# Kernel optimization log

Measured on AMD Instinct MI355X. Metric: run time of the kernel, lower is better.

Reference implementation:

```python
import jax, jax.numpy as jnp
import numpy as np

Q_DIM = 2048
HEADS = 16
HEAD_DIM = 128
INNER = HEADS * HEAD_DIM          # 2048
MLP_HID = int(Q_DIM * 4.0)        # 8192
MLP_MULT = 2
EPS = 1e-05
B, S = 2, 2048


def setup_inputs() -> dict:
    key = jax.random.key(0)
    ks = jax.random.split(key, 4)
    hidden_states = jax.random.normal(ks[0], (B, S, Q_DIM), dtype=jnp.float32)
    # interleaved RoPE tables: cos/sin of shape [S, HEAD_DIM]
    half = HEAD_DIM // 2
    freqs = 1.0 / (10000.0 ** (np.arange(half, dtype=np.float64) / half))
    ang = np.outer(np.arange(S, dtype=np.float64), freqs)      # [S, half]
    ang = np.repeat(ang, 2, axis=-1)                            # [S, HEAD_DIM]
    rope_cos = jnp.asarray(np.cos(ang), dtype=jnp.float32)
    rope_sin = jnp.asarray(np.sin(ang), dtype=jnp.float32)
    fused_out = 3 * INNER + MLP_HID * MLP_MULT                  # 22528
    W_qkv_mlp = jax.random.normal(ks[1], (Q_DIM, fused_out), dtype=jnp.float32) * (Q_DIM ** -0.5)
    norm_q_w = jnp.ones((HEAD_DIM,), dtype=jnp.float32)
    norm_k_w = jnp.ones((HEAD_DIM,), dtype=jnp.float32)
    W_out = jax.random.normal(ks[2], (INNER + MLP_HID, Q_DIM), dtype=jnp.float32) * ((INNER + MLP_HID) ** -0.5)
    b_out = jnp.zeros((Q_DIM,), dtype=jnp.float32)
    return {"hidden_states": hidden_states, "rope_cos": rope_cos, "rope_sin": rope_sin,
            "W_qkv_mlp": W_qkv_mlp, "norm_q_w": norm_q_w, "norm_k_w": norm_k_w,
            "W_out": W_out, "b_out": b_out}


def _rms_norm(x, w):
    # RMSNorm over the last (head_dim) axis
    return x * jax.lax.rsqrt(jnp.mean(x * x, axis=-1, keepdims=True) + EPS) * w


def _apply_rope(x, cos, sin):
    # x: [B, S, H, D]; interleaved rotate-half (diffusers real-rope convention)
    xr = x.reshape(*x.shape[:-1], HEAD_DIM // 2, 2)
    rot = jnp.stack([-xr[..., 1], xr[..., 0]], axis=-1).reshape(x.shape)
    return x * cos[None, :, None, :] + rot * sin[None, :, None, :]


def reference(hidden_states, rope_cos, rope_sin, W_qkv_mlp, norm_q_w, norm_k_w, W_out, b_out):
    b, s, _ = hidden_states.shape
    proj = hidden_states @ W_qkv_mlp                              # [B,S,22528]
    qkv, mlp_h = jnp.split(proj, [3 * INNER], axis=-1)
    q, k, v = jnp.split(qkv, 3, axis=-1)
    q = q.reshape(b, s, HEADS, HEAD_DIM)
    k = k.reshape(b, s, HEADS, HEAD_DIM)
    v = v.reshape(b, s, HEADS, HEAD_DIM)
    q = _rms_norm(q, norm_q_w)
    k = _rms_norm(k, norm_k_w)
    q = _apply_rope(q, rope_cos, rope_sin)
    k = _apply_rope(k, rope_cos, rope_sin)
    scale = HEAD_DIM ** -0.5
    scores = jnp.einsum('bqhd,bkhd->bhqk', q, k) * scale          # [B,H,S,S]
    attn = jax.nn.softmax(scores, axis=-1)
    out_attn = jnp.einsum('bhqk,bkhd->bqhd', attn, v).reshape(b, s, INNER)
    m1, m2 = jnp.split(mlp_h, 2, axis=-1)                         # SwiGLU
    mlp_out = jax.nn.silu(m1) * m2                                # [B,S,MLP_HID]
    cat = jnp.concatenate([out_attn, mlp_out], axis=-1)           # [B,S,INNER+MLP_HID]
    return cat @ W_out + b_out
```

## Files before the change

kernel.cpp:

```cpp
#include <hip/hip_runtime.h>

typedef unsigned short u16;
typedef unsigned int u32;
typedef __bf16 bf16x8 __attribute__((ext_vector_type(8)));
typedef float f32x4 __attribute__((ext_vector_type(4)));

#define MFMA16(a, b, c) __builtin_amdgcn_mfma_f32_16x16x32_bf16((a), (b), (c), 0, 0, 0)

#define S_LEN 2048
#define D_HEAD 128
#define NHEADS 16
#define NBH 32
#define QDIM 2048
#define NPROJ 22528
#define NCAT 10240
#define MROWS 4096

__device__ __forceinline__ float bf2f(u16 u) { return __uint_as_float(((u32)u) << 16); }
__device__ __forceinline__ u16 f2bf(float f) {
  u32 u = __float_as_uint(f);
  return (u16)((u + 0x7FFFu + ((u >> 16) & 1u)) >> 16);
}
__device__ __forceinline__ void gld16(const void* g, void* l) {
  __builtin_amdgcn_global_load_lds((__attribute__((address_space(1))) void*)(g),
                                   (__attribute__((address_space(3))) void*)(l), 16, 0, 0);
}

__global__ __launch_bounds__(256) void f32_to_bf16(const float* __restrict__ in,
                                                   u16* __restrict__ out) {
  const u32 i = blockIdx.x * 256 + threadIdx.x;
  const float4 v = ((const float4*)in)[i];
  uint2 o;
  o.x = (u32)f2bf(v.x) | ((u32)f2bf(v.y) << 16);
  o.y = (u32)f2bf(v.z) | ((u32)f2bf(v.w) << 16);
  ((uint2*)out)[i] = o;
}

__global__ __launch_bounds__(256) void transpose_f32_bf16(const float* __restrict__ in,
                                                          u16* __restrict__ out, int R, int C) {
  __shared__ u16 tile[64][65];
  const int tx = threadIdx.x & 63;
  const int ty = threadIdx.x >> 6;
  const int c0 = blockIdx.x * 64;
  const int r0 = blockIdx.y * 64;
#pragma unroll
  for (int it = 0; it < 16; ++it) {
    const int rr = ty * 16 + it;
    tile[rr][tx] = f2bf(in[(size_t)(r0 + rr) * C + c0 + tx]);
  }
  __syncthreads();
#pragma unroll
  for (int it = 0; it < 16; ++it) {
    const int rr = ty * 16 + it;
    out[(size_t)(c0 + rr) * R + r0 + tx] = tile[tx][rr];
  }
}

__global__ __launch_bounds__(256) void transpose_bf16_b(const u16* __restrict__ in,
                                                        u16* __restrict__ out, int R, int C) {
  __shared__ u16 tile[64][65];
  const int z = blockIdx.z;
  in += (size_t)z * R * C;
  out += (size_t)z * R * C;
  const int tx = threadIdx.x & 63;
  const int ty = threadIdx.x >> 6;
  const int c0 = blockIdx.x * 64;
  const int r0 = blockIdx.y * 64;
#pragma unroll
  for (int it = 0; it < 16; ++it) {
    const int rr = ty * 16 + it;
    tile[rr][tx] = in[(size_t)(r0 + rr) * C + c0 + tx];
  }
  __syncthreads();
#pragma unroll
  for (int it = 0; it < 16; ++it) {
    const int rr = ty * 16 + it;
    out[(size_t)(c0 + rr) * R + r0 + tx] = tile[tx][rr];
  }
}

template <int OUTF32>
__global__ __launch_bounds__(256, 2) void gemm_bt(const u16* __restrict__ A,
                                                  const u16* __restrict__ Bt,
                                                  void* __restrict__ Cvoid,
                                                  const float* __restrict__ bias, int N, int K) {
  __shared__ u16 As[128 * 64];
  __shared__ u16 Bs[128 * 64];
  const int t = threadIdx.x;
  const int l = t & 63;
  const int w = t >> 6;
  const int lr = l & 15;
  const int lg = l >> 4;
  const int m0 = blockIdx.y * 128;
  const int n0 = blockIdx.x * 128;
  const int wm = (w >> 1) * 64;
  const int wn = (w & 1) * 64;

  f32x4 acc[4][4] = {};
  const int obase = w * 1024 + l * 16;

  for (int k0 = 0; k0 < K; k0 += 64) {
#pragma unroll
    for (int rnd = 0; rnd < 4; ++rnd) {
      const int o = obase + rnd * 4096;
      const int row = o >> 7;
      const int g = (o & 127) >> 4;
      const int gs = g ^ (row & 7);
      gld16(A + (size_t)(m0 + row) * K + k0 + gs * 8, &As[rnd * 2048 + w * 512]);
      gld16(Bt + (size_t)(n0 + row) * K + k0 + gs * 8, &Bs[rnd * 2048 + w * 512]);
    }
    __syncthreads();

    bf16x8 af[4][2], bfr[4][2];
#pragma unroll
    for (int i = 0; i < 4; ++i) {
#pragma unroll
      for (int kc = 0; kc < 2; ++kc) {
        const int ra = wm + i * 16 + lr;
        af[i][kc] = *(const bf16x8*)&As[ra * 64 + (((kc * 4 + lg) ^ (ra & 7)) * 8)];
        const int rb = wn + i * 16 + lr;
        bfr[i][kc] = *(const bf16x8*)&Bs[rb * 64 + (((kc * 4 + lg) ^ (rb & 7)) * 8)];
      }
    }
#pragma unroll
    for (int kc = 0; kc < 2; ++kc)
#pragma unroll
      for (int i = 0; i < 4; ++i)
#pragma unroll
        for (int j = 0; j < 4; ++j)
          acc[i][j] = MFMA16(af[i][kc], bfr[j][kc], acc[i][j]);
    __syncthreads();
  }

  if (OUTF32) {
    float* C = (float*)Cvoid;
#pragma unroll
    for (int i = 0; i < 4; ++i)
#pragma unroll
      for (int j = 0; j < 4; ++j)
#pragma unroll
        for (int r = 0; r < 4; ++r) {
          const int row = m0 + wm + i * 16 + lg * 4 + r;
          const int col = n0 + wn + j * 16 + lr;
          C[(size_t)row * N + col] = acc[i][j][r] + bias[col];
        }
  } else {
    u16* C = (u16*)Cvoid;
#pragma unroll
    for (int i = 0; i < 4; ++i)
#pragma unroll
      for (int j = 0; j < 4; ++j)
#pragma unroll
        for (int r = 0; r < 4; ++r) {
          const int row = m0 + wm + i * 16 + lg * 4 + r;
          const int col = n0 + wn + j * 16 + lr;
          C[(size_t)row * N + col] = f2bf(acc[i][j][r]);
        }
  }
}

__global__ __launch_bounds__(256) void norm_rope(const u16* __restrict__ proj,
                                                 const float* __restrict__ cosT,
                                                 const float* __restrict__ sinT,
                                                 const float* __restrict__ wq,
                                                 const float* __restrict__ wk,
                                                 u16* __restrict__ Qb, u16* __restrict__ Kb,
                                                 u16* __restrict__ Vb) {
  const int l = threadIdx.x & 63;
  const int wg = blockIdx.x * 4 + (threadIdx.x >> 6);
  const int h = wg & 15;
  const int r = wg >> 4;
  const int b = r >> 11;
  const int s = r & 2047;
  const int bh = (b << 4) + h;

  const u16* p = proj + (size_t)r * NPROJ + h * 128 + 2 * l;
  const u32 qu = *(const u32*)(p);
  const u32 ku = *(const u32*)(p + QDIM);
  const u32 vu = *(const u32*)(p + 2 * QDIM);

  const float q0 = bf2f(qu & 0xffff), q1 = bf2f(qu >> 16);
  const float k0 = bf2f(ku & 0xffff), k1 = bf2f(ku >> 16);

  float sq = q0 * q0 + q1 * q1;
  float sk = k0 * k0 + k1 * k1;
#pragma unroll
  for (int m = 1; m < 64; m <<= 1) {
    sq += __shfl_xor(sq, m);
    sk += __shfl_xor(sk, m);
  }
  const float scq = rsqrtf(sq * (1.0f / 128.0f) + 1e-5f);
  const float sck = rsqrtf(sk * (1.0f / 128.0f) + 1e-5f);

  const float2 cc = *(const float2*)&cosT[s * 128 + 2 * l];
  const float2 ssn = *(const float2*)&sinT[s * 128 + 2 * l];
  const float w0 = wq[2 * l], w1 = wq[2 * l + 1];
  const float x0 = wk[2 * l], x1 = wk[2 * l + 1];

  const float qn0 = q0 * scq * w0, qn1 = q1 * scq * w1;
  const float kn0 = k0 * sck * x0, kn1 = k1 * sck * x1;

  const float ATT = 0.08838834764831845f;
  const float qr0 = (qn0 * cc.x - qn1 * ssn.x) * ATT;
  const float qr1 = (qn1 * cc.y + qn0 * ssn.y) * ATT;
  const float kr0 = kn0 * cc.x - kn1 * ssn.x;
  const float kr1 = kn1 * cc.y + kn0 * ssn.y;

  const size_t dst = ((size_t)bh * S_LEN + s) * 128 + 2 * l;
  *(u32*)(Qb + dst) = (u32)f2bf(qr0) | ((u32)f2bf(qr1) << 16);
  *(u32*)(Kb + dst) = (u32)f2bf(kr0) | ((u32)f2bf(kr1) << 16);
  *(u32*)(Vb + dst) = vu;
}

__global__ __launch_bounds__(256) void swiglu(const u16* __restrict__ proj,
                                              u16* __restrict__ Cat) {
  const u32 i = blockIdx.x * 256 + threadIdx.x;
  const u32 r = i >> 11;
  const u32 c = (i & 2047) * 4;
  const u16* p1 = proj + (size_t)r * NPROJ + 3 * QDIM + c;
  const uint2 a = *(const uint2*)p1;
  const uint2 bv = *(const uint2*)(p1 + 8192);
  const float a0 = bf2f(a.x & 0xffff), a1 = bf2f(a.x >> 16);
  const float a2 = bf2f(a.y & 0xffff), a3 = bf2f(a.y >> 16);
  const float b0 = bf2f(bv.x & 0xffff), b1 = bf2f(bv.x >> 16);
  const float b2 = bf2f(bv.y & 0xffff), b3 = bf2f(bv.y >> 16);
  const float o0 = a0 / (1.f + __expf(-a0)) * b0;
  const float o1 = a1 / (1.f + __expf(-a1)) * b1;
  const float o2 = a2 / (1.f + __expf(-a2)) * b2;
  const float o3 = a3 / (1.f + __expf(-a3)) * b3;
  uint2 o;
  o.x = (u32)f2bf(o0) | ((u32)f2bf(o1) << 16);
  o.y = (u32)f2bf(o2) | ((u32)f2bf(o3) << 16);
  *(uint2*)(Cat + (size_t)r * NCAT + QDIM + c) = o;
}

__global__ __launch_bounds__(256, 2) void attn_fwd(const u16* __restrict__ Qb,
                                                   const u16* __restrict__ Kb,
                                                   const u16* __restrict__ Vt,
                                                   u16* __restrict__ Cat) {
  __shared__ u16 Ks[64 * 128];
  __shared__ u16 Vs[128 * 64];
  __shared__ u16 Ps[4][32 * 64];

  const int t = threadIdx.x;
  const int l = t & 63;
  const int w = t >> 6;
  const int lr = l & 15;
  const int lg = l >> 4;
  const int qt = blockIdx.x;
  const int bh = blockIdx.y;
  const int b = bh >> 4;
  const int h = bh & 15;
  const int q0 = qt * 128 + w * 32;

  bf16x8 qf[2][4];
#pragma unroll
  for (int im = 0; im < 2; ++im)
#pragma unroll
    for (int kc = 0; kc < 4; ++kc)
      qf[im][kc] =
          *(const bf16x8*)&Qb[((size_t)bh * S_LEN + q0 + im * 16 + lr) * 128 + kc * 32 + lg * 8];

  f32x4 oacc[2][8] = {};
  float mrun[2][4], lrun[2][4];
#pragma unroll
  for (int im = 0; im < 2; ++im)
#pragma unroll
    for (int r = 0; r < 4; ++r) {
      mrun[im][r] = -1e30f;
      lrun[im][r] = 0.f;
    }

  const int obase = w * 1024 + l * 16;
  u16* P = Ps[w];

  for (int kt = 0; kt < 32; ++kt) {
    const int kk0 = kt * 64;
#pragma unroll
    for (int rnd = 0; rnd < 4; ++rnd) {
      const int o = obase + rnd * 4096;
      {
        const int key = o >> 8;
        const int g = (o & 255) >> 4;
        const int gs = g ^ (key & 7);
        gld16(Kb + ((size_t)bh * S_LEN + kk0 + key) * 128 + gs * 8, &Ks[rnd * 2048 + w * 512]);
      }
      {
        const int d = o >> 7;
        const int g = (o & 127) >> 4;
        const int gs = g ^ (d & 7);
        gld16(Vt + ((size_t)bh * 128 + d) * S_LEN + kk0 + gs * 8, &Vs[rnd * 2048 + w * 512]);
      }
    }
    __syncthreads();

    f32x4 sf[2][4] = {};
#pragma unroll
    for (int j = 0; j < 4; ++j) {
      const int kr = j * 16 + lr;
      bf16x8 kf[4];
#pragma unroll
      for (int kc = 0; kc < 4; ++kc)
        kf[kc] = *(const bf16x8*)&Ks[kr * 128 + (((kc * 4 + lg) ^ (kr & 7)) * 8)];
#pragma unroll
      for (int kc = 0; kc < 4; ++kc)
#pragma unroll
        for (int im = 0; im < 2; ++im)
          sf[im][j] = MFMA16(qf[im][kc], kf[kc], sf[im][j]);
    }

#pragma unroll
    for (int im = 0; im < 2; ++im) {
#pragma unroll
      for (int r = 0; r < 4; ++r) {
        float v = fmaxf(fmaxf(sf[im][0][r], sf[im][1][r]), fmaxf(sf[im][2][r], sf[im][3][r]));
        v = fmaxf(v, __shfl_xor(v, 1));
        v = fmaxf(v, __shfl_xor(v, 2));
        v = fmaxf(v, __shfl_xor(v, 4));
        v = fmaxf(v, __shfl_xor(v, 8));
        const float mnew = fmaxf(mrun[im][r], v);
        const float alpha = __expf(mrun[im][r] - mnew);
        mrun[im][r] = mnew;
        float psum = 0.f;
#pragma unroll
        for (int j = 0; j < 4; ++j) {
          const float pv = __expf(sf[im][j][r] - mnew);
          sf[im][j][r] = pv;
          psum += pv;
        }
        psum += __shfl_xor(psum, 1);
        psum += __shfl_xor(psum, 2);
        psum += __shfl_xor(psum, 4);
        psum += __shfl_xor(psum, 8);
        lrun[im][r] = lrun[im][r] * alpha + psum;
#pragma unroll
        for (int df = 0; df < 8; ++df) oacc[im][df][r] *= alpha;
      }
    }

#pragma unroll
    for (int im = 0; im < 2; ++im)
#pragma unroll
      for (int j = 0; j < 4; ++j)
#pragma unroll
        for (int r = 0; r < 4; ++r) {
          const int q = im * 16 + lg * 4 + r;
          const int key = j * 16 + lr;
          const int g = key >> 3;
          P[q * 64 + ((g ^ (q & 7)) * 8) + (key & 7)] = f2bf(sf[im][j][r]);
        }

#pragma unroll
    for (int kc = 0; kc < 2; ++kc) {
      bf16x8 pa[2];
#pragma unroll
      for (int im = 0; im < 2; ++im) {
        const int q = im * 16 + lr;
        pa[im] = *(const bf16x8*)&P[q * 64 + (((kc * 4 + lg) ^ (q & 7)) * 8)];
      }
#pragma unroll
      for (int df = 0; df < 8; ++df) {
        const int d = df * 16 + lr;
        const bf16x8 vb = *(const bf16x8*)&Vs[d * 64 + (((kc * 4 + lg) ^ (d & 7)) * 8)];
#pragma unroll
        for (int im = 0; im < 2; ++im) oacc[im][df] = MFMA16(pa[im], vb, oacc[im][df]);
      }
    }
    __syncthreads();
  }

#pragma unroll
  for (int im = 0; im < 2; ++im)
#pragma unroll
    for (int r = 0; r < 4; ++r) {
      const float inv = 1.0f / lrun[im][r];
      const int row = b * S_LEN + q0 + im * 16 + lg * 4 + r;
#pragma unroll
      for (int df = 0; df < 8; ++df) {
        const int col = h * 128 + df * 16 + lr;
        Cat[(size_t)row * NCAT + col] = f2bf(oacc[im][df][r] * inv);
      }
    }
}

extern "C" void kernel_launch(void* const* d_in, const int* in_sizes, int n_in, void* d_out,
                              int out_size, void* d_ws, size_t ws_size, hipStream_t stream) {
  (void)in_sizes; (void)n_in; (void)out_size; (void)ws_size;
  const float* hs = (const float*)d_in[0];
  const float* rcos = (const float*)d_in[1];
  const float* rsin = (const float*)d_in[2];
  const float* Wqkv = (const float*)d_in[3];
  const float* wq = (const float*)d_in[4];
  const float* wk = (const float*)d_in[5];
  const float* Wout = (const float*)d_in[6];
  const float* bout = (const float*)d_in[7];
  float* out = (float*)d_out;

  char* ws = (char*)d_ws;
  size_t off = 0;
  auto nxt = [&](size_t bytes) {
    char* p = ws + off;
    off += (bytes + 255) & ~(size_t)255;
    return p;
  };
  u16* Xb = (u16*)nxt((size_t)MROWS * QDIM * 2);
  u16* Wqkvt = (u16*)nxt((size_t)NPROJ * QDIM * 2);
  u16* Woutt = (u16*)nxt((size_t)QDIM * NCAT * 2);
  u16* proj = (u16*)nxt((size_t)MROWS * NPROJ * 2);
  u16* Qb = (u16*)nxt((size_t)NBH * S_LEN * D_HEAD * 2);
  u16* Kb = (u16*)nxt((size_t)NBH * S_LEN * D_HEAD * 2);
  u16* Vb = (u16*)nxt((size_t)NBH * S_LEN * D_HEAD * 2);
  u16* Vt = (u16*)nxt((size_t)NBH * S_LEN * D_HEAD * 2);
  u16* Cat = (u16*)nxt((size_t)MROWS * NCAT * 2);

  f32_to_bf16<<<(MROWS * QDIM / 4) / 256, 256, 0, stream>>>(hs, Xb);
  transpose_f32_bf16<<<dim3(NPROJ / 64, QDIM / 64), 256, 0, stream>>>(Wqkv, Wqkvt, QDIM, NPROJ);
  transpose_f32_bf16<<<dim3(QDIM / 64, NCAT / 64), 256, 0, stream>>>(Wout, Woutt, NCAT, QDIM);

  gemm_bt<0><<<dim3(NPROJ / 128, MROWS / 128), 256, 0, stream>>>(Xb, Wqkvt, proj, nullptr,
                                                                 NPROJ, QDIM);
  norm_rope<<<MROWS * NHEADS / 4, 256, 0, stream>>>(proj, rcos, rsin, wq, wk, Qb, Kb, Vb);
  transpose_bf16_b<<<dim3(D_HEAD / 64, S_LEN / 64, NBH), 256, 0, stream>>>(Vb, Vt, S_LEN, D_HEAD);

  swiglu<<<(MROWS * 8192 / 4) / 256, 256, 0, stream>>>(proj, Cat);

  attn_fwd<<<dim3(S_LEN / 128, NBH), 256, 0, stream>>>(Qb, Kb, Vt, Cat);

  gemm_bt<1><<<dim3(QDIM / 128, MROWS / 128), 256, 0, stream>>>(Cat, Woutt, out, bout,
                                                                QDIM, NCAT);
}
```

Before: 913.9 us.

## Add 256x256 double-buffered ping-pong GEMM for QKV/MLP projection with XCD swizzle

Replaces the 128x128 projection GEMM with a new 512-thread 256x256-tile kernel. It double-buffers LDS, prefetches two k-tiles ahead, and interleaves LDS fragment reads and global loads with MFMA phases separated by barriers and setprio. Both GEMMs also get a block-index swizzle across the 8 XCDs to improve L2 locality. The larger tiles raise data reuse and overlap memory with compute, at the cost of more LDS (128KB per block, which limits occupancy) and fragile hand-placed waitcnt and barrier ordering.

```diff
diff --git a/kernel.cpp b/kernel.cpp
--- a/kernel.cpp
+++ b/kernel.cpp
@@ -15,6 +15,12 @@
 #define NPROJ 22528
 #define NCAT 10240
 #define MROWS 4096
+
+#define BARRIER() __builtin_amdgcn_s_barrier()
+#define SCHEDB() __builtin_amdgcn_sched_barrier(0)
+#define WAITLGKM() asm volatile("s_waitcnt lgkmcnt(0)" ::: "memory")
+#define WAITVM8() asm volatile("s_waitcnt vmcnt(8)" ::: "memory")
+#define WAITVM0() asm volatile("s_waitcnt vmcnt(0)" ::: "memory")
 
 __device__ __forceinline__ float bf2f(u16 u) { return __uint_as_float(((u32)u) << 16); }
 __device__ __forceinline__ u16 f2bf(float f) {
@@ -79,11 +85,165 @@
   }
 }
 
+
+__device__ __forceinline__ void stage_tile(const u16* __restrict__ src, int ldk,
+                                           u16* ldsbase, int k0, int t) {
+  const int w64 = t & ~63;
+#pragma unroll
+  for (int j = 0; j < 4; ++j) {
+    const int o = (j * 512 + t) * 16;
+    const int row = o >> 7;
+    const int g = (o & 127) >> 4;
+    const int gs = g ^ (row & 7);
+    gld16(src + (size_t)row * ldk + k0 + gs * 8, ldsbase + (((j * 512 + w64) * 16) >> 1));
+  }
+}
+
+__device__ __forceinline__ bf16x8 rdfrag(const u16* lds, int row, int kc, int lg) {
+  return *(const bf16x8*)&lds[row * 64 + (((kc * 4 + lg) ^ (row & 7)) << 3)];
+}
+
+__global__ __launch_bounds__(512, 2) void gemm256(const u16* __restrict__ A,
+                                                  const u16* __restrict__ Bt,
+                                                  u16* __restrict__ C, int N, int K,
+                                                  int nbm) {
+  __shared__ u16 As[2][256 * 64];
+  __shared__ u16 Bs[2][256 * 64];
+  const int t = threadIdx.x;
+  const int l = t & 63;
+  const int w = t >> 6;
+  const int lr = l & 15;
+  const int lg = l >> 4;
+  const int wm = (w >> 2) * 128;
+  const int wn = (w & 3) * 64;
+
+  const int nwg = gridDim.x;
+  const int cpx = nwg >> 3;
+  const int swz = (blockIdx.x & 7) * cpx + (blockIdx.x >> 3);
+  const int bm = swz % nbm;
+  const int bn = swz / nbm;
+  const u16* Ab = A + (size_t)(bm * 256) * K;
+  const u16* Bb = Bt + (size_t)(bn * 256) * K;
+  const int NT = K >> 6;
+
+  f32x4 acc[8][4] = {};
+
+  stage_tile(Bb, K, &Bs[0][0], 0, t);
+  stage_tile(Ab, K, &As[0][0], 0, t);
+  stage_tile(Bb, K, &Bs[1][0], 64, t);
+  stage_tile(Ab, K, &As[1][0], 64, t);
+  WAITVM8();
+  BARRIER();
+
+  for (int kt = 0; kt < NT; ++kt) {
+    const int d = kt & 1;
+    const u16* Al = &As[d][0];
+    const u16* Bl = &Bs[d][0];
+    const bool pre = (kt + 2 < NT);
+    bf16x8 a_[4][2], b01[2][2], b23[2][2];
+
+#pragma unroll
+    for (int i = 0; i < 4; ++i)
+#pragma unroll
+      for (int kc = 0; kc < 2; ++kc) a_[i][kc] = rdfrag(Al, wm + i * 16 + lr, kc, lg);
+#pragma unroll
+    for (int j = 0; j < 2; ++j)
+#pragma unroll
+      for (int kc = 0; kc < 2; ++kc) b01[j][kc] = rdfrag(Bl, wn + j * 16 + lr, kc, lg);
+    BARRIER();
+    SCHEDB();
+    WAITLGKM();
+    __builtin_amdgcn_s_setprio(1);
+#pragma unroll
+    for (int kc = 0; kc < 2; ++kc)
+#pragma unroll
+      for (int i = 0; i < 4; ++i)
+#pragma unroll
+        for (int j = 0; j < 2; ++j) acc[i][j] = MFMA16(a_[i][kc], b01[j][kc], acc[i][j]);
+    __builtin_amdgcn_s_setprio(0);
+    SCHEDB();
+    BARRIER();
+
+#pragma unroll
+    for (int j = 0; j < 2; ++j)
+#pragma unroll
+      for (int kc = 0; kc < 2; ++kc) b23[j][kc] = rdfrag(Bl, wn + 32 + j * 16 + lr, kc, lg);
+    BARRIER();
+    SCHEDB();
+    WAITLGKM();
+    __builtin_amdgcn_s_setprio(1);
+#pragma unroll
+    for (int kc = 0; kc < 2; ++kc)
+#pragma unroll
+      for (int i = 0; i < 4; ++i)
+#pragma unroll
+        for (int j = 0; j < 2; ++j)
+          acc[i][2 + j] = MFMA16(a_[i][kc], b23[j][kc], acc[i][2 + j]);
+    __builtin_amdgcn_s_setprio(0);
+    SCHEDB();
+    BARRIER();
+
+#pragma unroll
+    for (int i = 0; i < 4; ++i)
+#pragma unroll
+      for (int kc = 0; kc < 2; ++kc) a_[i][kc] = rdfrag(Al, wm + 64 + i * 16 + lr, kc, lg);
+    if (pre) stage_tile(Bb, K, &Bs[d][0], (kt + 2) * 64, t);
+    BARRIER();
+    SCHEDB();
+    WAITLGKM();
+    __builtin_amdgcn_s_setprio(1);
+#pragma unroll
+    for (int kc = 0; kc < 2; ++kc)
+#pragma unroll
+      for (int i = 0; i < 4; ++i)
+#pragma unroll
+        for (int j = 0; j < 2; ++j)
+          acc[4 + i][2 + j] = MFMA16(a_[i][kc], b23[j][kc], acc[4 + i][2 + j]);
+    __builtin_amdgcn_s_setprio(0);
+    SCHEDB();
+    BARRIER();
+
+    if (pre) stage_tile(Ab, K, &As[d][0], (kt + 2) * 64, t);
+    BARRIER();
+    SCHEDB();
+    __builtin_amdgcn_s_setprio(1);
+#pragma unroll
+    for (int kc = 0; kc < 2; ++kc)
+#pragma unroll
+      for (int i = 0; i < 4; ++i)
+#pragma unroll
+        for (int j = 0; j < 2; ++j)
+          acc[4 + i][j] = MFMA16(a_[i][kc], b01[j][kc], acc[4 + i][j]);
+    __builtin_amdgcn_s_setprio(0);
+    SCHEDB();
+    if (pre) {
+      WAITVM8();
+    } else {
+      WAITVM0();
+    }
+    BARRIER();
+  }
+
+  const int m0 = bm * 256 + wm;
+  const int n0 = bn * 256 + wn;
+#pragma unroll
+  for (int i = 0; i < 8; ++i)
+#pragma unroll
+    for (int j = 0; j < 4; ++j)
+#pragma unroll
+      for (int r = 0; r < 4; ++r) {
+        const int row = m0 + i * 16 + lg * 4 + r;
+        const int col = n0 + j * 16 + lr;
+        C[(size_t)row * N + col] = f2bf(acc[i][j][r]);
+      }
+}
+
 template <int OUTF32>
 __global__ __launch_bounds__(256, 2) void gemm_bt(const u16* __restrict__ A,
                                                   const u16* __restrict__ Bt,
                                                   void* __restrict__ Cvoid,
-                                                  const float* __restrict__ bias, int N, int K) {
+                                                  const float* __restrict__ bias, int N, int K,
+                                                  int nbn) {
   __shared__ u16 As[128 * 64];
   __shared__ u16 Bs[128 * 64];
   const int t = threadIdx.x;
@@ -91,8 +251,13 @@
   const int w = t >> 6;
   const int lr = l & 15;
   const int lg = l >> 4;
-  const int m0 = blockIdx.y * 128;
-  const int n0 = blockIdx.x * 128;
+  const int nwg = gridDim.x;
+  const int cpx = nwg >> 3;
+  const int swz = (blockIdx.x & 7) * cpx + (blockIdx.x >> 3);
+  const int bm = swz / nbn;
+  const int bn = swz % nbn;
+  const int m0 = bm * 128;
+  const int n0 = bn * 128;
   const int wm = (w >> 1) * 64;
   const int wn = (w & 1) * 64;
 
@@ -417,8 +582,9 @@
   transpose_f32_bf16<<<dim3(NPROJ / 64, QDIM / 64), 256, 0, stream>>>(Wqkv, Wqkvt, QDIM, NPROJ);
   transpose_f32_bf16<<<dim3(QDIM / 64, NCAT / 64), 256, 0, stream>>>(Wout, Woutt, NCAT, QDIM);
 
-  gemm_bt<0><<<dim3(NPROJ / 128, MROWS / 128), 256, 0, stream>>>(Xb, Wqkvt, proj, nullptr,
-                                                                 NPROJ, QDIM);
+  gemm256<<<(MROWS / 256) * (NPROJ / 256), 512, 0, stream>>>(Xb, Wqkvt, proj, NPROJ, QDIM,
+                                                             MROWS / 256);
+
   norm_rope<<<MROWS * NHEADS / 4, 256, 0, stream>>>(proj, rcos, rsin, wq, wk, Qb, Kb, Vb);
   transpose_bf16_b<<<dim3(D_HEAD / 64, S_LEN / 64, NBH), 256, 0, stream>>>(Vb, Vt, S_LEN, D_HEAD);
 
@@ -426,6 +592,6 @@
 
   attn_fwd<<<dim3(S_LEN / 128, NBH), 256, 0, stream>>>(Qb, Kb, Vt, Cat);
 
-  gemm_bt<1><<<dim3(QDIM / 128, MROWS / 128), 256, 0, stream>>>(Cat, Woutt, out, bout,
-                                                                QDIM, NCAT);
-}
+  gemm_bt<1><<<(MROWS / 128) * (QDIM / 128), 256, 0, stream>>>(Cat, Woutt, out, bout, QDIM,
+                                                               NCAT, QDIM / 128);
+}
```

Result: slower. 943.9 us (+3.3%).

## Double-buffer attention K/V loads and swizzle GEMM block order across XCDs

Applied to the files above, without the earlier changes.

The attention kernel now double-buffers K and V tiles in shared memory. It prefetches the next tile while computing on the current one, and replaces the per-iteration syncthreads pairs with a vmcnt wait plus a single barrier, raising MFMA priority via setprio. Both GEMMs switch to a 1D grid with an XCD-aware block swizzle and a column- or row-major tile order, to improve L2 reuse of the shared operand. Double-buffering doubles the K/V LDS footprint, to about 80KB per block, which may limit occupancy to one block per CU.

```diff
diff --git a/kernel.cpp b/kernel.cpp
--- a/kernel.cpp
+++ b/kernel.cpp
@@ -15,6 +15,9 @@
 #define NPROJ 22528
 #define NCAT 10240
 #define MROWS 4096
+
+#define BARRIER() __builtin_amdgcn_s_barrier()
+#define WAITVM0() asm volatile("s_waitcnt vmcnt(0)" ::: "memory")
 
 __device__ __forceinline__ float bf2f(u16 u) { return __uint_as_float(((u32)u) << 16); }
 __device__ __forceinline__ u16 f2bf(float f) {
@@ -79,11 +82,12 @@
   }
 }
 
-template <int OUTF32>
+template <int OUTF32, int COLMAJ>
 __global__ __launch_bounds__(256, 2) void gemm_bt(const u16* __restrict__ A,
                                                   const u16* __restrict__ Bt,
                                                   void* __restrict__ Cvoid,
-                                                  const float* __restrict__ bias, int N, int K) {
+                                                  const float* __restrict__ bias, int N, int K,
+                                                  int nb) {
   __shared__ u16 As[128 * 64];
   __shared__ u16 Bs[128 * 64];
   const int t = threadIdx.x;
@@ -91,8 +95,13 @@
   const int w = t >> 6;
   const int lr = l & 15;
   const int lg = l >> 4;
-  const int m0 = blockIdx.y * 128;
-  const int n0 = blockIdx.x * 128;
+  const int nwg = gridDim.x;
+  const int cpx = nwg >> 3;
+  const int swz = (blockIdx.x & 7) * cpx + (blockIdx.x >> 3);
+  const int bm = COLMAJ ? (swz % nb) : (swz / nb);
+  const int bn = COLMAJ ? (swz / nb) : (swz % nb);
+  const int m0 = bm * 128;
+  const int n0 = bn * 128;
   const int wm = (w >> 1) * 64;
   const int wn = (w & 1) * 64;
 
@@ -238,8 +247,8 @@
                                                    const u16* __restrict__ Kb,
                                                    const u16* __restrict__ Vt,
                                                    u16* __restrict__ Cat) {
-  __shared__ u16 Ks[64 * 128];
-  __shared__ u16 Vs[128 * 64];
+  __shared__ u16 Ks[2][64 * 128];
+  __shared__ u16 Vs[2][128 * 64];
   __shared__ u16 Ps[4][32 * 64];
 
   const int t = threadIdx.x;
@@ -252,6 +261,10 @@
   const int b = bh >> 4;
   const int h = bh & 15;
   const int q0 = qt * 128 + w * 32;
+  const int obase = w * 1024 + l * 16;
+
+  const size_t kbase = (size_t)bh * S_LEN * 128;
+  const size_t vbase = (size_t)bh * 128 * S_LEN;
 
   bf16x8 qf[2][4];
 #pragma unroll
@@ -271,11 +284,10 @@
       lrun[im][r] = 0.f;
     }
 
-  const int obase = w * 1024 + l * 16;
   u16* P = Ps[w];
 
-  for (int kt = 0; kt < 32; ++kt) {
-    const int kk0 = kt * 64;
+  auto stageKV = [&](int buf, int kt2) {
+    const int kk0 = kt2 * 64;
 #pragma unroll
     for (int rnd = 0; rnd < 4; ++rnd) {
       const int o = obase + rnd * 4096;
@@ -283,31 +295,46 @@
         const int key = o >> 8;
         const int g = (o & 255) >> 4;
         const int gs = g ^ (key & 7);
-        gld16(Kb + ((size_t)bh * S_LEN + kk0 + key) * 128 + gs * 8, &Ks[rnd * 2048 + w * 512]);
+        gld16(Kb + kbase + (size_t)(kk0 + key) * 128 + gs * 8,
+              &Ks[buf][rnd * 2048 + w * 512]);
       }
       {
         const int d = o >> 7;
         const int g = (o & 127) >> 4;
         const int gs = g ^ (d & 7);
-        gld16(Vt + ((size_t)bh * 128 + d) * S_LEN + kk0 + gs * 8, &Vs[rnd * 2048 + w * 512]);
-      }
-    }
-    __syncthreads();
+        gld16(Vt + vbase + (size_t)d * S_LEN + kk0 + gs * 8,
+              &Vs[buf][rnd * 2048 + w * 512]);
+      }
+    }
+  };
+
+  stageKV(0, 0);
+  WAITVM0();
+  BARRIER();
+
+  int cur = 0;
+  for (int kt = 0; kt < 32; ++kt) {
+    if (kt + 1 < 32) stageKV(cur ^ 1, kt + 1);
+
+    const u16* Kc = &Ks[cur][0];
+    const u16* Vc = &Vs[cur][0];
 
     f32x4 sf[2][4] = {};
+    __builtin_amdgcn_s_setprio(1);
 #pragma unroll
     for (int j = 0; j < 4; ++j) {
       const int kr = j * 16 + lr;
       bf16x8 kf[4];
 #pragma unroll
       for (int kc = 0; kc < 4; ++kc)
-        kf[kc] = *(const bf16x8*)&Ks[kr * 128 + (((kc * 4 + lg) ^ (kr & 7)) * 8)];
+        kf[kc] = *(const bf16x8*)&Kc[kr * 128 + (((kc * 4 + lg) ^ (kr & 7)) * 8)];
 #pragma unroll
       for (int kc = 0; kc < 4; ++kc)
 #pragma unroll
         for (int im = 0; im < 2; ++im)
           sf[im][j] = MFMA16(qf[im][kc], kf[kc], sf[im][j]);
     }
+    __builtin_amdgcn_s_setprio(0);
 
 #pragma unroll
     for (int im = 0; im < 2; ++im) {
@@ -350,6 +377,7 @@
           P[q * 64 + ((g ^ (q & 7)) * 8) + (key & 7)] = f2bf(sf[im][j][r]);
         }
 
+    __builtin_amdgcn_s_setprio(1);
 #pragma unroll
     for (int kc = 0; kc < 2; ++kc) {
       bf16x8 pa[2];
@@ -361,12 +389,16 @@
 #pragma unroll
       for (int df = 0; df < 8; ++df) {
         const int d = df * 16 + lr;
-        const bf16x8 vb = *(const bf16x8*)&Vs[d * 64 + (((kc * 4 + lg) ^ (d & 7)) * 8)];
+        const bf16x8 vb = *(const bf16x8*)&Vc[d * 64 + (((kc * 4 + lg) ^ (d & 7)) * 8)];
 #pragma unroll
         for (int im = 0; im < 2; ++im) oacc[im][df] = MFMA16(pa[im], vb, oacc[im][df]);
       }
     }
-    __syncthreads();
+    __builtin_amdgcn_s_setprio(0);
+
+    WAITVM0();
+    BARRIER();
+    cur ^= 1;
   }
 
 #pragma unroll
@@ -417,8 +449,9 @@
   transpose_f32_bf16<<<dim3(NPROJ / 64, QDIM / 64), 256, 0, stream>>>(Wqkv, Wqkvt, QDIM, NPROJ);
   transpose_f32_bf16<<<dim3(QDIM / 64, NCAT / 64), 256, 0, stream>>>(Wout, Woutt, NCAT, QDIM);
 
-  gemm_bt<0><<<dim3(NPROJ / 128, MROWS / 128), 256, 0, stream>>>(Xb, Wqkvt, proj, nullptr,
-                                                                 NPROJ, QDIM);
+  gemm_bt<0, 1><<<(MROWS / 128) * (NPROJ / 128), 256, 0, stream>>>(Xb, Wqkvt, proj, nullptr,
+                                                                   NPROJ, QDIM, MROWS / 128);
+
   norm_rope<<<MROWS * NHEADS / 4, 256, 0, stream>>>(proj, rcos, rsin, wq, wk, Qb, Kb, Vb);
   transpose_bf16_b<<<dim3(D_HEAD / 64, S_LEN / 64, NBH), 256, 0, stream>>>(Vb, Vt, S_LEN, D_HEAD);
 
@@ -426,6 +459,6 @@
 
   attn_fwd<<<dim3(S_LEN / 128, NBH), 256, 0, stream>>>(Qb, Kb, Vt, Cat);
 
-  gemm_bt<1><<<dim3(QDIM / 128, MROWS / 128), 256, 0, stream>>>(Cat, Woutt, out, bout,
-                                                                QDIM, NCAT);
-}
+  gemm_bt<1, 0><<<(MROWS / 128) * (QDIM / 128), 256, 0, stream>>>(Cat, Woutt, out, bout, QDIM,
+                                                                  NCAT, QDIM / 128);
+}
```

Result: slower. 933.7 us (+2.2%).
